# Performance work log

Measured on AMD Instinct MI355X. Metric: run time of the kernel, lower is better.

The kernel has to match this reference:

```python
import jax, jax.numpy as jnp
import numpy as np

B, C, H, W = 8, 256, 128, 128
WS, NH = 8, 8
HD = C // NH
HID = 4 * C
EPS = 1e-5


def _dwconv(x, w, b, pad):
    # x: [B,C,H,W], w: [C,1,k,k] depthwise
    y = jax.lax.conv_general_dilated(
        x, w, window_strides=(1, 1), padding=[(pad, pad), (pad, pad)],
        feature_group_count=C, dimension_numbers=('NCHW', 'OIHW', 'NCHW'))
    return y + b[None, :, None, None]


def _ln(x, g, b):
    m = jnp.mean(x, axis=-1, keepdims=True)
    v = jnp.mean(jnp.square(x - m), axis=-1, keepdims=True)
    return (x - m) * jax.lax.rsqrt(v + EPS) * g + b


def _mha(x, wqkv, bqkv, wo, bo):
    # x: [N,L,C]; torch nn.MultiheadAttention with q=k=v=x
    N, L, _ = x.shape
    qkv = x @ wqkv.T + bqkv
    q, k, v = jnp.split(qkv, 3, axis=-1)
    q = q.reshape(N, L, NH, HD)
    k = k.reshape(N, L, NH, HD)
    v = v.reshape(N, L, NH, HD)
    scale = HD ** -0.5
    a = jnp.einsum('nqhd,nkhd->nhqk', q * scale, k)
    a = jax.nn.softmax(a, axis=-1)
    o = jnp.einsum('nhqk,nkhd->nqhd', a, v).reshape(N, L, C)
    return o @ wo.T + bo


def _window_partition(x):
    b, c, h, w = x.shape
    x = x.reshape(b, c, h // WS, WS, w // WS, WS)
    return jnp.transpose(x, (0, 2, 4, 3, 5, 1)).reshape(-1, WS, WS, c)


def _window_reverse(win, h, w):
    c = win.shape[-1]
    x = win.reshape(-1, h // WS, w // WS, WS, WS, c)
    return jnp.transpose(x, (0, 5, 1, 3, 2, 4)).reshape(-1, c, h, w)


def _grid_partition(x):
    b, c, h, w = x.shape
    x = x.reshape(b, c, WS, h // WS, WS, w // WS)
    return jnp.transpose(x, (0, 3, 5, 2, 4, 1)).reshape(-1, WS, WS, c)


def _grid_reverse(grid, h, w):
    c = grid.shape[-1]
    x = grid.reshape(-1, h // WS, w // WS, WS, WS, c)
    return jnp.transpose(x, (0, 5, 2, 1, 3, 4)).reshape(-1, c, h, w)


def setup_inputs() -> dict:
    key = jax.random.key(0)
    ks = jax.random.split(key, 32)
    n = lambda k, s, sc=0.02: jax.random.normal(k, s, jnp.float32) * sc
    z = lambda s: jnp.zeros(s, jnp.float32)
    return {
        'x': jax.random.normal(ks[0], (B, C, H, W), jnp.float32),
        'w1': n(ks[1], (C, 1, 3, 3)), 'b1': z((C,)),
        'w2': n(ks[2], (C, 1, 5, 5)), 'b2': z((C,)),
        'w3': n(ks[3], (C, 1, 7, 7)), 'b3': z((C,)),
        'wf': n(ks[4], (C, 3 * C)), 'bf': z((C,)),
        'gw': jnp.ones((C,), jnp.float32), 'bw': z((C,)),
        'wqkv_w': n(ks[5], (3 * C, C)), 'bqkv_w': z((3 * C,)),
        'wo_w': n(ks[6], (C, C)), 'bo_w': z((C,)),
        'gg': jnp.ones((C,), jnp.float32), 'bg': z((C,)),
        'wqkv_g': n(ks[7], (3 * C, C)), 'bqkv_g': z((3 * C,)),
        'wo_g': n(ks[8], (C, C)), 'bo_g': z((C,)),
        'gm': jnp.ones((C,), jnp.float32), 'bm': z((C,)),
        'm1w': n(ks[9], (HID, C)), 'm1b': z((HID,)),
        'm2w': n(ks[10], (C, HID)), 'm2b': z((C,)),
    }


def reference(x, w1, b1, w2, b2, w3, b3, wf, bf, gw, bw, wqkv_w, bqkv_w, wo_w, bo_w,
              gg, bg, wqkv_g, bqkv_g, wo_g, bo_g, gm, bm, m1w, m1b, m2w, m2b):
    s1 = _dwconv(x, w1, b1, 1)
    s2 = _dwconv(x, w2, b2, 2)
    s3 = _dwconv(x, w3, b3, 3)
    cat = jnp.concatenate([s1, s2, s3], axis=1)  # [B,3C,H,W]
    x_multi = jnp.einsum('bkhw,ck->bchw', cat, wf) + bf[None, :, None, None]

    # window attention branch
    xw = _window_partition(x_multi).reshape(-1, WS * WS, C)
    xw = _ln(xw, gw, bw)
    xw = _mha(xw, wqkv_w, bqkv_w, wo_w, bo_w).reshape(-1, WS, WS, C)
    x = x + _window_reverse(xw, H, W)

    # grid attention branch
    xg = _grid_partition(x).reshape(-1, WS * WS, C)
    xg = _ln(xg, gg, bg)
    xg = _mha(xg, wqkv_g, bqkv_g, wo_g, bo_g).reshape(-1, WS, WS, C)
    x = x + _grid_reverse(xg, H, W)

    # MLP over flattened tokens
    xf = x.reshape(B, C, H * W).transpose(0, 2, 1)  # [B,HW,C]
    h = _ln(xf, gm, bm)
    h = jax.nn.gelu(h @ m1w.T + m1b, approximate=False)
    h = h @ m2w.T + m2b
    xf = xf + h
    return xf.transpose(0, 2, 1).reshape(B, C, H, W)
```

## Files before the change

kernel.cpp:

```cpp
#include <hip/hip_runtime.h>
#include <hip/hip_bf16.h>
#include <math.h>


#define CC 256
#define HH 128
#define WW 128
#define HWSZ 16384

typedef __attribute__((ext_vector_type(8))) short short8v;
typedef __attribute__((ext_vector_type(4))) float float4v;

#if defined(__has_builtin)
#if __has_builtin(__builtin_amdgcn_global_load_lds)
#define USE_GLDS 1
#endif
#endif
#ifndef USE_GLDS
#define USE_GLDS 0
#endif

static __device__ __forceinline__ float bf2f(unsigned short u) {
    union { float f; unsigned int i; } x; x.i = ((unsigned int)u) << 16; return x.f;
}
static __device__ __forceinline__ unsigned short f2bf(float f) {
    union { float f; unsigned int i; } x; x.f = f;
    unsigned int r = x.i + 0x7FFFu + ((x.i >> 16) & 1u);
    return (unsigned short)(r >> 16);
}
template<int FMT> static __device__ __forceinline__ float ldin(const void* p, size_t i) {
    if (FMT == 0) return bf2f(((const unsigned short*)p)[i]);
    return ((const float*)p)[i];
}

#if USE_GLDS
static __device__ __forceinline__ void gload16(const unsigned short* g, unsigned short* l) {
    __builtin_amdgcn_global_load_lds(
        (const __attribute__((address_space(1))) unsigned int*)g,
        (__attribute__((address_space(3))) unsigned int*)l, 16, 0, 0);
}
#endif

__global__ void probe_kernel(const unsigned short* x, int* flags) {
    __shared__ int mx[256];
    int m = 0;
    for (int i = threadIdx.x; i < 65536; i += 256) {
        int e = (x[i] >> 7) & 0xFF;
        m = m > e ? m : e;
    }
    mx[threadIdx.x] = m; __syncthreads();
    for (int s = 128; s > 0; s >>= 1) {
        if (threadIdx.x < s) mx[threadIdx.x] = mx[threadIdx.x] > mx[threadIdx.x + s] ? mx[threadIdx.x] : mx[threadIdx.x + s];
        __syncthreads();
    }
    if (threadIdx.x == 0) flags[0] = (mx[0] > 200) ? 1 : 0;
}
__global__ void report_ws_kernel(unsigned short* out, long long n, float code) {
    long long i = (long long)blockIdx.x * blockDim.x + threadIdx.x;
    const long long st = (long long)gridDim.x * blockDim.x;
    unsigned short c = f2bf(code);
    for (; i < n; i += st) out[i] = c;
}

#define WF_OFF   0
#define WQW_OFF  196608
#define WOW_OFF  393216
#define WQG_OFF  458752
#define WOG_OFF  655360
#define M1W_OFF  720896
#define M2W_OFF  983040
#define WTOT     1245184
#define BF_OFF   0
#define GW_OFF   256
#define BW_OFF   512
#define BQW_OFF  768
#define BOW_OFF  1536
#define GG_OFF   1792
#define BG_OFF   2048
#define BQG_OFF  2304
#define BOG_OFF  3072
#define GM_OFF   3328
#define BM_OFF   3584
#define M1B_OFF  3840
#define M2B_OFF  4864
#define BTOT     5120

template<int FMT>
__global__ __launch_bounds__(256) void convert_weights_kernel(
    const void* __restrict__ wf, const void* __restrict__ wqkv_w, const void* __restrict__ wo_w,
    const void* __restrict__ wqkv_g, const void* __restrict__ wo_g,
    const void* __restrict__ m1w, const void* __restrict__ m2w,
    unsigned short* __restrict__ out, const int* __restrict__ flags)
{
    if (flags[0] != FMT) return;
    int i = blockIdx.x * 256 + threadIdx.x;
    const int st = gridDim.x * 256;
    for (; i < WTOT; i += st) {
        const void* src; int off;
        if (i < WQW_OFF)      { src = wf;     off = i; }
        else if (i < WOW_OFF) { src = wqkv_w; off = i - WQW_OFF; }
        else if (i < WQG_OFF) { src = wo_w;   off = i - WOW_OFF; }
        else if (i < WOG_OFF) { src = wqkv_g; off = i - WQG_OFF; }
        else if (i < M1W_OFF) { src = wo_g;   off = i - WOG_OFF; }
        else if (i < M2W_OFF) { src = m1w;    off = i - M1W_OFF; }
        else                  { src = m2w;    off = i - M2W_OFF; }
        out[i] = (FMT == 0) ? ((const unsigned short*)src)[off]
                            : f2bf(((const float*)src)[off]);
    }
}

template<int FMT>
__global__ __launch_bounds__(256) void convert_bias_kernel(
    const void* bf_, const void* gw, const void* bw, const void* bqkv_w, const void* bo_w,
    const void* gg, const void* bg, const void* bqkv_g, const void* bo_g,
    const void* gm, const void* bm, const void* m1b, const void* m2b,
    float* __restrict__ out, const int* __restrict__ flags)
{
    if (flags[0] != FMT) return;
    int i = blockIdx.x * 256 + threadIdx.x;
    if (i >= BTOT) return;
    const void* src; int off;
    if (i < GW_OFF)        { src = bf_;    off = i; }
    else if (i < BW_OFF)   { src = gw;     off = i - GW_OFF; }
    else if (i < BQW_OFF)  { src = bw;     off = i - BW_OFF; }
    else if (i < BOW_OFF)  { src = bqkv_w; off = i - BQW_OFF; }
    else if (i < GG_OFF)   { src = bo_w;   off = i - BOW_OFF; }
    else if (i < BG_OFF)   { src = gg;     off = i - GG_OFF; }
    else if (i < BQG_OFF)  { src = bg;     off = i - BG_OFF; }
    else if (i < BOG_OFF)  { src = bqkv_g; off = i - BQG_OFF; }
    else if (i < GM_OFF)   { src = bo_g;   off = i - BOG_OFF; }
    else if (i < BM_OFF)   { src = gm;     off = i - GM_OFF; }
    else if (i < M1B_OFF)  { src = bm;     off = i - BM_OFF; }
    else if (i < M2B_OFF)  { src = m1b;    off = i - M1B_OFF; }
    else                   { src = m2b;    off = i - M2B_OFF; }
    out[i] = ldin<FMT>(src, off);
}

template<int FMT>
__global__ __launch_bounds__(256) void transpose_in_kernel(
    const void* __restrict__ in, float* __restrict__ out, const int* __restrict__ flags)
{
    if (flags[0] != FMT) return;
    __shared__ float tile[64][65];
    const int b  = blockIdx.z;
    const int s0 = blockIdx.x * 64;
    const int r0 = blockIdx.y * 64;
    const int tx = threadIdx.x & 63;
    const int ty = threadIdx.x >> 6;
    const size_t sb = (size_t)b * CC * HWSZ;
    float* dst = out + (size_t)b * HWSZ * CC;
#pragma unroll
    for (int rr = 0; rr < 16; ++rr) {
        int row = ty + rr * 4;
        tile[row][tx] = ldin<FMT>(in, sb + (size_t)(r0 + row) * HWSZ + s0 + tx);
    }
    __syncthreads();
#pragma unroll
    for (int rr = 0; rr < 16; ++rr) {
        int srow = ty + rr * 4;
        dst[(size_t)(s0 + srow) * CC + r0 + tx] = tile[tx][srow];
    }
}

template<int FMT>
__global__ __launch_bounds__(256) void transpose_out_kernel(
    const float* __restrict__ in, void* __restrict__ out, const int* __restrict__ flags)
{
    if (flags[0] != FMT) return;
    __shared__ float tile[64][65];
    const int b  = blockIdx.z;
    const int h0 = blockIdx.x * 64;
    const int c0 = blockIdx.y * 64;
    const int tx = threadIdx.x & 63;
    const int ty = threadIdx.x >> 6;
    const float* src = in + (size_t)b * HWSZ * CC;
    const size_t db = (size_t)b * CC * HWSZ;
#pragma unroll
    for (int rr = 0; rr < 16; ++rr) {
        int row = ty + rr * 4;
        tile[row][tx] = src[(size_t)(h0 + row) * CC + c0 + tx];
    }
    __syncthreads();
#pragma unroll
    for (int rr = 0; rr < 16; ++rr) {
        int crow = ty + rr * 4;
        size_t di = db + (size_t)(c0 + crow) * HWSZ + h0 + tx;
        float v = tile[tx][crow];
        if (FMT) ((float*)out)[di] = v;
        else ((unsigned short*)out)[di] = f2bf(v);
    }
}

template<int FMT>
__global__ __launch_bounds__(256) void dwconv_cat_kernel(
    const void* __restrict__ x,
    const void* __restrict__ w1, const void* __restrict__ b1,
    const void* __restrict__ w2, const void* __restrict__ b2,
    const void* __restrict__ w3, const void* __restrict__ b3,
    unsigned short* __restrict__ cat, int Mc, const int* __restrict__ flags)
{
    if (flags[0] != FMT) return;
    __shared__ float patch[14][140];
    __shared__ float wt[83];
    const int hb = blockIdx.x;
    const int c  = blockIdx.y;
    const int b  = blockIdx.z;
    const int tid = threadIdx.x;

    if (tid < 83) {
        float v;
        if (tid < 9)       v = ldin<FMT>(w1, c * 9 + tid);
        else if (tid < 34) v = ldin<FMT>(w2, c * 25 + (tid - 9));
        else               v = ldin<FMT>(w3, c * 49 + (tid - 34));
        wt[tid] = v;
    }
    const int h0 = hb * 8;
    const size_t xb = ((size_t)b * CC + c) * HWSZ;

    for (int i = tid; i < 448; i += 256) {
        const int r  = i >> 5;
        const int c4 = (i & 31) * 4;
        const int gh = h0 - 3 + r;
        float4 vv;
        if (gh >= 0 && gh < HH) {
            if (FMT == 0) {
                ushort4 u = *(const ushort4*)((const unsigned short*)x + xb + (size_t)gh * WW + c4);
                vv.x = bf2f(u.x); vv.y = bf2f(u.y); vv.z = bf2f(u.z); vv.w = bf2f(u.w);
            } else {
                vv = *(const float4*)((const float*)x + xb + (size_t)gh * WW + c4);
            }
        } else { vv.x = vv.y = vv.z = vv.w = 0.f; }
        *(float4*)&patch[r][c4 + 4] = vv;
    }
    for (int i = tid; i < 84; i += 256) {
        const int r = i / 6, j = i % 6;
        const int gh = h0 - 3 + r;
        const int gw = (j < 3) ? (j - 3) : (125 + j);
        float v = 0.f;
        if (gh >= 0 && gh < HH && gw >= 0 && gw < WW)
            v = ldin<FMT>(x, xb + (size_t)gh * WW + gw);
        patch[r][gw + 4] = v;
    }
    __syncthreads();

    const int w  = tid & 127;
    const int rb = (tid >> 7) * 4;
    const float bb1 = ldin<FMT>(b1, c), bb2 = ldin<FMT>(b2, c), bb3 = ldin<FMT>(b3, c);

#pragma unroll
    for (int ri = 0; ri < 4; ++ri) {
        const int row = rb + ri;
        const int pr  = row + 3;
        float s1 = bb1, s2 = bb2, s3 = bb3;
#pragma unroll
        for (int dy = -1; dy <= 1; ++dy)
#pragma unroll
            for (int dx = -1; dx <= 1; ++dx)
                s1 += patch[pr + dy][w + 4 + dx] * wt[(dy + 1) * 3 + (dx + 1)];
#pragma unroll
        for (int dy = -2; dy <= 2; ++dy)
#pragma unroll
            for (int dx = -2; dx <= 2; ++dx)
                s2 += patch[pr + dy][w + 4 + dx] * wt[9 + (dy + 2) * 5 + (dx + 2)];
#pragma unroll
        for (int dy = -3; dy <= 3; ++dy)
#pragma unroll
            for (int dx = -3; dx <= 3; ++dx)
                s3 += patch[pr + dy][w + 4 + dx] * wt[34 + (dy + 3) * 7 + (dx + 3)];

        const size_t m = (size_t)b * HWSZ + (size_t)(h0 + row) * WW + w;
        cat[(size_t)c * Mc + m]         = f2bf(s1);
        cat[(size_t)(256 + c) * Mc + m] = f2bf(s2);
        cat[(size_t)(512 + c) * Mc + m] = f2bf(s3);
    }
}

template<int ALAYOUT, int EPI>
__global__ __launch_bounds__(256) void gemm_mfma_kernel(
    const unsigned short* __restrict__ A, const unsigned short* __restrict__ Bw,
    const float* __restrict__ bias, void* __restrict__ Cout,
    int N, int K, int lda)
{
    constexpr int ASTR = ALAYOUT ? 72 : 64;
    __shared__ unsigned short As[128 * ASTR];
    __shared__ unsigned short Bs[128 * 64];
    const int tid  = threadIdx.x;
    const int lane = tid & 63;
    const int wv   = tid >> 6;
    const int wm   = (wv >> 1) * 64;
    const int wn   = (wv & 1) * 64;
    const int l15  = lane & 15;
    const int quad = lane >> 4;

    const int nbx = gridDim.x;
    const int nwg = nbx * gridDim.y;
    const int bid = blockIdx.y * nbx + blockIdx.x;
    const int swz = (bid & 7) * (nwg >> 3) + (bid >> 3);
    const int m0 = (swz / nbx) * 128;
    const int n0 = (swz % nbx) * 128;

    const int sr   = lane >> 3;
    const int scol = (lane & 7) * 8;

    float4v acc[4][4] = {};

    for (int k0 = 0; k0 < K; k0 += 64) {
        __syncthreads();
        if (ALAYOUT == 0) {
            const unsigned short* ga = A + (size_t)(m0 + wv * 32 + sr) * K + k0 + scol;
#pragma unroll
            for (int p = 0; p < 4; ++p) {
                unsigned short* lb = &As[(wv * 32 + p * 8) * 64];
#if USE_GLDS
                gload16(ga + (size_t)(p * 8) * K, lb);
#else
                *(short8v*)(lb + lane * 8) = *(const short8v*)(ga + (size_t)(p * 8) * K);
#endif
            }
        } else {
#pragma unroll
            for (int p = 0; p < 4; ++p) {
                const int k  = p * 16 + (tid >> 4);
                const int mm = (tid & 15) * 8;
                const unsigned short* g = A + (size_t)(k0 + k) * lda + m0 + mm;
                ushort4 va = *(const ushort4*)g;
                ushort4 vb = *(const ushort4*)(g + 4);
                As[(mm + 0) * 72 + k] = va.x; As[(mm + 1) * 72 + k] = va.y;
                As[(mm + 2) * 72 + k] = va.z; As[(mm + 3) * 72 + k] = va.w;
                As[(mm + 4) * 72 + k] = vb.x; As[(mm + 5) * 72 + k] = vb.y;
                As[(mm + 6) * 72 + k] = vb.z; As[(mm + 7) * 72 + k] = vb.w;
            }
        }
        {
            const unsigned short* gb = Bw + (size_t)(n0 + wv * 32 + sr) * K + k0 + scol;
#pragma unroll
            for (int p = 0; p < 4; ++p) {
                unsigned short* lb = &Bs[(wv * 32 + p * 8) * 64];
#if USE_GLDS
                gload16(gb + (size_t)(p * 8) * K, lb);
#else
                *(short8v*)(lb + lane * 8) = *(const short8v*)(gb + (size_t)(p * 8) * K);
#endif
            }
        }
#if USE_GLDS
        asm volatile("s_waitcnt vmcnt(0)" ::: "memory");
#endif
        __syncthreads();

#pragma unroll
        for (int ks = 0; ks < 64; ks += 32) {
            short8v af[4], bfv[4];
#pragma unroll
            for (int i = 0; i < 4; ++i)
                af[i] = *(const short8v*)&As[(wm + i * 16 + l15) * ASTR + ks + quad * 8];
#pragma unroll
            for (int i = 0; i < 4; ++i)
                bfv[i] = *(const short8v*)&Bs[(wn + i * 16 + l15) * 64 + ks + quad * 8];
#pragma unroll
            for (int mi = 0; mi < 4; ++mi)
#pragma unroll
                for (int ni = 0; ni < 4; ++ni)
                    acc[mi][ni] = __builtin_amdgcn_mfma_f32_16x16x32_bf16(
                        af[mi], bfv[ni], acc[mi][ni], 0, 0, 0);
        }
    }

    float bv[4];
#pragma unroll
    for (int ni = 0; ni < 4; ++ni) bv[ni] = bias[n0 + wn + ni * 16 + l15];

#pragma unroll
    for (int mi = 0; mi < 4; ++mi) {
#pragma unroll
        for (int r = 0; r < 4; ++r) {
            const size_t row = (size_t)(m0 + wm + mi * 16 + quad * 4 + r);
#pragma unroll
            for (int ni = 0; ni < 4; ++ni) {
                const int col = n0 + wn + ni * 16 + l15;
                float v = acc[mi][ni][r] + bv[ni];
                if (EPI == 0) {
                    ((unsigned short*)Cout)[row * N + col] = f2bf(v);
                } else if (EPI == 1) {
                    float g = 0.5f * v * (1.0f + erff(v * 0.70710678118654752f));
                    ((unsigned short*)Cout)[row * N + col] = f2bf(g);
                } else {
                    ((float*)Cout)[row * N + col] += v;
                }
            }
        }
    }
}

template<int FIN>
__global__ __launch_bounds__(256) void ln_kernel(
    const void* __restrict__ inv, const float* __restrict__ g,
    const float* __restrict__ b, unsigned short* __restrict__ out)
{
    const int lane = threadIdx.x & 63;
    const int wv   = threadIdx.x >> 6;
    const size_t m = (size_t)blockIdx.x * 4 + wv;
    const int c0 = lane * 4;
    float v[4];
    if (FIN == 0) {
        ushort4 u = *(const ushort4*)((const unsigned short*)inv + m * CC + c0);
        v[0] = bf2f(u.x); v[1] = bf2f(u.y); v[2] = bf2f(u.z); v[3] = bf2f(u.w);
    } else {
        float4 f = *(const float4*)((const float*)inv + m * CC + c0);
        v[0] = f.x; v[1] = f.y; v[2] = f.z; v[3] = f.w;
    }
    float s  = v[0] + v[1] + v[2] + v[3];
    float sq = v[0]*v[0] + v[1]*v[1] + v[2]*v[2] + v[3]*v[3];
#pragma unroll
    for (int off = 32; off > 0; off >>= 1) {
        s  += __shfl_xor(s,  off);
        sq += __shfl_xor(sq, off);
    }
    const float mean = s * 0.00390625f;
    float var = sq * 0.00390625f - mean * mean;
    if (var < 0.f) var = 0.f;
    const float rs = rsqrtf(var + 1e-5f);
    ushort4 o;
    o.x = f2bf((v[0] - mean) * rs * g[c0 + 0] + b[c0 + 0]);
    o.y = f2bf((v[1] - mean) * rs * g[c0 + 1] + b[c0 + 1]);
    o.z = f2bf((v[2] - mean) * rs * g[c0 + 2] + b[c0 + 2]);
    o.w = f2bf((v[3] - mean) * rs * g[c0 + 3] + b[c0 + 3]);
    *(ushort4*)(out + m * CC + c0) = o;
}

template<int MODE>
__global__ __launch_bounds__(256) void attn_kernel(
    const unsigned short* __restrict__ qkv, unsigned short* __restrict__ attn_out)
{
    __shared__ unsigned short q_lds[64 * 72];
    __shared__ unsigned short k_lds[64 * 72];
    __shared__ unsigned short v_lds[64 * 72];
    __shared__ unsigned short vt_lds[32 * 72];
    __shared__ unsigned short p_lds[64 * 72];

    const int tid  = threadIdx.x;
    const int lane = tid & 63;
    const int wv   = tid >> 6;
    const int l15  = lane & 15;
    const int quad = lane >> 4;
    const int wi   = blockIdx.x;
    const int b    = wi >> 8;
    const int rem  = wi & 255;
    const int i2   = rem >> 4;
    const int j2   = rem & 15;

    const float scale = 0.17677669529663687f;

    auto gt_read = [&](int tok) -> size_t {
        const int p = tok >> 3, qq = tok & 7;
        int h_r, w_r;
        if (MODE == 0) { h_r = i2 * 8 + p;  w_r = j2 * 8 + qq; }
        else           { h_r = p * 16 + i2; w_r = qq * 16 + j2; }
        return (size_t)b * HWSZ + (size_t)h_r * WW + w_r;
    };
    auto gt_write = [&](int tok) -> size_t {
        const int p = tok >> 3, qq = tok & 7;
        int h_w, w_w;
        if (MODE == 0) { h_w = i2 * 8 + p; w_w = j2 * 8 + qq; }
        else { h_w = j2 * 8 + (i2 >> 1); w_w = (i2 & 1) * 64 + p * 8 + qq; }
        return (size_t)b * HWSZ + (size_t)h_w * WW + w_w;
    };

    for (int g = 0; g < 4; ++g) {
        for (int v = tid; v < 512; v += 256) {
            const int tok = v >> 3;
            const int cg  = (v & 7) * 8;
            const unsigned short* src = qkv + gt_read(tok) * 768 + g * 64 + cg;
            *(short8v*)&q_lds[tok * 72 + cg] = *(const short8v*)(src);
            *(short8v*)&k_lds[tok * 72 + cg] = *(const short8v*)(src + 256);
            *(short8v*)&v_lds[tok * 72 + cg] = *(const short8v*)(src + 512);
        }
        __syncthreads();

#pragma unroll
        for (int hl = 0; hl < 2; ++hl) {
            {
                const int tok = lane;
                const int dg  = wv * 8;
                short8v vv = *(const short8v*)&v_lds[tok * 72 + hl * 32 + dg];
#pragma unroll
                for (int j = 0; j < 8; ++j)
                    vt_lds[(dg + j) * 72 + tok] = (unsigned short)vv[j];
            }

            short8v af = *(const short8v*)&q_lds[(16 * wv + l15) * 72 + hl * 32 + quad * 8];
            float4v s[4];
#pragma unroll
            for (int ni = 0; ni < 4; ++ni) {
                short8v bfv = *(const short8v*)&k_lds[(16 * ni + l15) * 72 + hl * 32 + quad * 8];
                float4v z = {};
                s[ni] = __builtin_amdgcn_mfma_f32_16x16x32_bf16(af, bfv, z, 0, 0, 0);
            }

#pragma unroll
            for (int r = 0; r < 4; ++r) {
                float m1 = fmaxf(fmaxf(s[0][r], s[1][r]), fmaxf(s[2][r], s[3][r]));
#pragma unroll
                for (int off = 1; off < 16; off <<= 1) m1 = fmaxf(m1, __shfl_xor(m1, off));
                const float rowmax = m1 * scale;
                float sum = 0.f;
#pragma unroll
                for (int ni = 0; ni < 4; ++ni) {
                    const float e = __expf(s[ni][r] * scale - rowmax);
                    s[ni][r] = e; sum += e;
                }
#pragma unroll
                for (int off = 1; off < 16; off <<= 1) sum += __shfl_xor(sum, off);
                const float inv = 1.f / sum;
#pragma unroll
                for (int ni = 0; ni < 4; ++ni) s[ni][r] *= inv;
            }

#pragma unroll
            for (int ni = 0; ni < 4; ++ni)
#pragma unroll
                for (int r = 0; r < 4; ++r)
                    p_lds[(16 * wv + quad * 4 + r) * 72 + ni * 16 + l15] = f2bf(s[ni][r]);

            __syncthreads();

            float4v o[2] = {};
#pragma unroll
            for (int kk = 0; kk < 2; ++kk) {
                short8v pf = *(const short8v*)&p_lds[(16 * wv + l15) * 72 + kk * 32 + quad * 8];
#pragma unroll
                for (int dt = 0; dt < 2; ++dt) {
                    short8v vf = *(const short8v*)&vt_lds[(dt * 16 + l15) * 72 + kk * 32 + quad * 8];
                    o[dt] = __builtin_amdgcn_mfma_f32_16x16x32_bf16(pf, vf, o[dt], 0, 0, 0);
                }
            }

            const int head = g * 2 + hl;
#pragma unroll
            for (int r = 0; r < 4; ++r) {
                const int tok = 16 * wv + quad * 4 + r;
                unsigned short* op = attn_out + gt_write(tok) * CC + head * 32;
                op[l15]      = f2bf(o[0][r]);
                op[16 + l15] = f2bf(o[1][r]);
            }
            __syncthreads();
        }
    }
}

extern "C" void kernel_launch(void* const* d_in, const int* in_sizes, int n_in,
                              void* d_out, int out_size, void* d_ws, size_t ws_size,
                              hipStream_t stream)
{
    const void* x      = d_in[0];
    const void* w1     = d_in[1];  const void* b1  = d_in[2];
    const void* w2     = d_in[3];  const void* b2  = d_in[4];
    const void* w3     = d_in[5];  const void* b3  = d_in[6];
    const void* wf     = d_in[7];  const void* bf_ = d_in[8];
    const void* gw     = d_in[9];  const void* bw  = d_in[10];
    const void* wqkv_w = d_in[11]; const void* bqkv_w = d_in[12];
    const void* wo_w   = d_in[13]; const void* bo_w   = d_in[14];
    const void* gg     = d_in[15]; const void* bg  = d_in[16];
    const void* wqkv_g = d_in[17]; const void* bqkv_g = d_in[18];
    const void* wo_g   = d_in[19]; const void* bo_g   = d_in[20];
    const void* gm     = d_in[21]; const void* bm  = d_in[22];
    const void* m1w    = d_in[23]; const void* m1b = d_in[24];
    const void* m2w    = d_in[25]; const void* m2b = d_in[26];

    const size_t MiB = 1048576ull;
    const long long nout = (long long)out_size;

    if (72 * MiB > ws_size) {
        float wsMiB = (float)(ws_size / MiB);
        if (wsMiB > 8192.f) wsMiB = 8192.f;
        report_ws_kernel<<<1024, 256, 0, stream>>>((unsigned short*)d_out, nout, 1024.f + wsMiB);
        return;
    }

    int nb = 8;
    while (nb > 1 && (size_t)nb * 64 * MiB + 8 * MiB > ws_size) nb >>= 1;
    const int nchunks = 8 / nb;
    const int Mc = nb * HWSZ;

    char* ws = (char*)d_ws;
    float*          xs   = (float*)ws;
    unsigned short* regA = (unsigned short*)(ws + (size_t)nb * 16 * MiB);
    unsigned short* xmat = (unsigned short*)(ws + (size_t)nb * 48 * MiB);
    unsigned short* xln  = (unsigned short*)(ws + (size_t)nb * 56 * MiB);
    int*            flags = (int*)(ws + (size_t)nb * 64 * MiB);
    unsigned short* wbf  = (unsigned short*)(ws + (size_t)nb * 64 * MiB + 1 * MiB);
    float*          bcv  = (float*)(ws + (size_t)nb * 64 * MiB + 4 * MiB);

    probe_kernel<<<1, 256, 0, stream>>>((const unsigned short*)x, flags);
    convert_weights_kernel<0><<<1024, 256, 0, stream>>>(wf, wqkv_w, wo_w, wqkv_g, wo_g, m1w, m2w, wbf, flags);
    convert_weights_kernel<1><<<1024, 256, 0, stream>>>(wf, wqkv_w, wo_w, wqkv_g, wo_g, m1w, m2w, wbf, flags);
    convert_bias_kernel<0><<<20, 256, 0, stream>>>(bf_, gw, bw, bqkv_w, bo_w, gg, bg, bqkv_g, bo_g, gm, bm, m1b, m2b, bcv, flags);
    convert_bias_kernel<1><<<20, 256, 0, stream>>>(bf_, gw, bw, bqkv_w, bo_w, gg, bg, bqkv_g, bo_g, gm, bm, m1b, m2b, bcv, flags);

    const int MB = Mc / 128;
    for (int c = 0; c < nchunks; ++c) {
        const size_t elemOff = (size_t)c * nb * CC * HWSZ;
        const void* xc0 = (const void*)((const unsigned short*)x + elemOff);
        const void* xc1 = (const void*)((const float*)x + elemOff);
        void* outc0 = (void*)((unsigned short*)d_out + elemOff);
        void* outc1 = (void*)((float*)d_out + elemOff);
        unsigned short* cat  = regA;
        unsigned short* qkvb = regA;
        unsigned short* h1   = regA;
        unsigned short* xm   = xmat;
        unsigned short* attn = xmat;

        transpose_in_kernel<0><<<dim3(256, 4, nb), 256, 0, stream>>>(xc0, xs, flags);
        transpose_in_kernel<1><<<dim3(256, 4, nb), 256, 0, stream>>>(xc1, xs, flags);

        dwconv_cat_kernel<0><<<dim3(16, 256, nb), 256, 0, stream>>>(xc0, w1, b1, w2, b2, w3, b3, cat, Mc, flags);
        dwconv_cat_kernel<1><<<dim3(16, 256, nb), 256, 0, stream>>>(xc1, w1, b1, w2, b2, w3, b3, cat, Mc, flags);

        gemm_mfma_kernel<1, 0><<<dim3(2, MB), 256, 0, stream>>>(cat, wbf + WF_OFF, bcv + BF_OFF, xm, 256, 768, Mc);

        ln_kernel<0><<<Mc / 4, 256, 0, stream>>>(xm, bcv + GW_OFF, bcv + BW_OFF, xln);
        gemm_mfma_kernel<0, 0><<<dim3(6, MB), 256, 0, stream>>>(xln, wbf + WQW_OFF, bcv + BQW_OFF, qkvb, 768, 256, 0);
        attn_kernel<0><<<nb * 256, 256, 0, stream>>>(qkvb, attn);
        gemm_mfma_kernel<0, 2><<<dim3(2, MB), 256, 0, stream>>>(attn, wbf + WOW_OFF, bcv + BOW_OFF, xs, 256, 256, 0);

        ln_kernel<1><<<Mc / 4, 256, 0, stream>>>(xs, bcv + GG_OFF, bcv + BG_OFF, xln);
        gemm_mfma_kernel<0, 0><<<dim3(6, MB), 256, 0, stream>>>(xln, wbf + WQG_OFF, bcv + BQG_OFF, qkvb, 768, 256, 0);
        attn_kernel<1><<<nb * 256, 256, 0, stream>>>(qkvb, attn);
        gemm_mfma_kernel<0, 2><<<dim3(2, MB), 256, 0, stream>>>(attn, wbf + WOG_OFF, bcv + BOG_OFF, xs, 256, 256, 0);

        ln_kernel<1><<<Mc / 4, 256, 0, stream>>>(xs, bcv + GM_OFF, bcv + BM_OFF, xln);
        gemm_mfma_kernel<0, 1><<<dim3(8, MB), 256, 0, stream>>>(xln, wbf + M1W_OFF, bcv + M1B_OFF, h1, 1024, 256, 0);
        gemm_mfma_kernel<0, 2><<<dim3(2, MB), 256, 0, stream>>>(h1, wbf + M2W_OFF, bcv + M2B_OFF, xs, 256, 1024, 0);

        transpose_out_kernel<0><<<dim3(256, 4, nb), 256, 0, stream>>>(xs, outc0, flags);
        transpose_out_kernel<1><<<dim3(256, 4, nb), 256, 0, stream>>>(xs, outc1, flags);
    }
}
```

Measured before the change: 1.842 ms.

## Register-block depthwise conv, vectorize transposes, preconvert dwconv weights to fp32 arena

The depthwise conv kernel now has each thread compute four adjacent outputs. It loads each 7-wide patch row once as float4 vectors and reuses those values across the 3x3, 5x5 and 7x7 filters, then writes ushort4 stores. Its weights and biases now come from a preconverted fp32 arena filled by the bias-conversion kernel, not from per-block shared-memory staging. The input and output transposes switch to 4-wide vector global loads and stores, which aims to cut memory instruction count. One risk is strided LDS accesses in the transposes, which may cause bank conflicts.

```diff
diff --git a/kernel.cpp b/kernel.cpp
--- a/kernel.cpp
+++ b/kernel.cpp
@@ -83,7 +83,13 @@
 #define BM_OFF   3584
 #define M1B_OFF  3840
 #define M2B_OFF  4864
-#define BTOT     5120
+#define DW1_OFF  5120
+#define DW2_OFF  7424
+#define DW3_OFF  13824
+#define DB1_OFF  26368
+#define DB2_OFF  26624
+#define DB3_OFF  26880
+#define BTOT     27136
 
 template<int FMT>
 __global__ __launch_bounds__(256) void convert_weights_kernel(
@@ -114,26 +120,36 @@
     const void* bf_, const void* gw, const void* bw, const void* bqkv_w, const void* bo_w,
     const void* gg, const void* bg, const void* bqkv_g, const void* bo_g,
     const void* gm, const void* bm, const void* m1b, const void* m2b,
+    const void* w1, const void* w2, const void* w3,
+    const void* b1, const void* b2, const void* b3,
     float* __restrict__ out, const int* __restrict__ flags)
 {
     if (flags[0] != FMT) return;
     int i = blockIdx.x * 256 + threadIdx.x;
-    if (i >= BTOT) return;
-    const void* src; int off;
-    if (i < GW_OFF)        { src = bf_;    off = i; }
-    else if (i < BW_OFF)   { src = gw;     off = i - GW_OFF; }
-    else if (i < BQW_OFF)  { src = bw;     off = i - BW_OFF; }
-    else if (i < BOW_OFF)  { src = bqkv_w; off = i - BQW_OFF; }
-    else if (i < GG_OFF)   { src = bo_w;   off = i - BOW_OFF; }
-    else if (i < BG_OFF)   { src = gg;     off = i - GG_OFF; }
-    else if (i < BQG_OFF)  { src = bg;     off = i - BG_OFF; }
-    else if (i < BOG_OFF)  { src = bqkv_g; off = i - BQG_OFF; }
-    else if (i < GM_OFF)   { src = bo_g;   off = i - BOG_OFF; }
-    else if (i < BM_OFF)   { src = gm;     off = i - GM_OFF; }
-    else if (i < M1B_OFF)  { src = bm;     off = i - BM_OFF; }
-    else if (i < M2B_OFF)  { src = m1b;    off = i - M1B_OFF; }
-    else                   { src = m2b;    off = i - M2B_OFF; }
-    out[i] = ldin<FMT>(src, off);
+    const int st = gridDim.x * 256;
+    for (; i < BTOT; i += st) {
+        const void* src; int off;
+        if (i < GW_OFF)        { src = bf_;    off = i; }
+        else if (i < BW_OFF)   { src = gw;     off = i - GW_OFF; }
+        else if (i < BQW_OFF)  { src = bw;     off = i - BW_OFF; }
+        else if (i < BOW_OFF)  { src = bqkv_w; off = i - BQW_OFF; }
+        else if (i < GG_OFF)   { src = bo_w;   off = i - BOW_OFF; }
+        else if (i < BG_OFF)   { src = gg;     off = i - GG_OFF; }
+        else if (i < BQG_OFF)  { src = bg;     off = i - BG_OFF; }
+        else if (i < BOG_OFF)  { src = bqkv_g; off = i - BQG_OFF; }
+        else if (i < GM_OFF)   { src = bo_g;   off = i - BOG_OFF; }
+        else if (i < BM_OFF)   { src = gm;     off = i - GM_OFF; }
+        else if (i < M1B_OFF)  { src = bm;     off = i - BM_OFF; }
+        else if (i < M2B_OFF)  { src = m1b;    off = i - M1B_OFF; }
+        else if (i < DW1_OFF)  { src = m2b;    off = i - M2B_OFF; }
+        else if (i < DW2_OFF)  { src = w1;     off = i - DW1_OFF; }
+        else if (i < DW3_OFF)  { src = w2;     off = i - DW2_OFF; }
+        else if (i < DB1_OFF)  { src = w3;     off = i - DW3_OFF; }
+        else if (i < DB2_OFF)  { src = b1;     off = i - DB1_OFF; }
+        else if (i < DB3_OFF)  { src = b2;     off = i - DB2_OFF; }
+        else                   { src = b3;     off = i - DB3_OFF; }
+        out[i] = ldin<FMT>(src, off);
+    }
 }
 
 template<int FMT>
@@ -149,10 +165,23 @@
     const int ty = threadIdx.x >> 6;
     const size_t sb = (size_t)b * CC * HWSZ;
     float* dst = out + (size_t)b * HWSZ * CC;
-#pragma unroll
-    for (int rr = 0; rr < 16; ++rr) {
-        int row = ty + rr * 4;
-        tile[row][tx] = ldin<FMT>(in, sb + (size_t)(r0 + row) * HWSZ + s0 + tx);
+
+    const int hw4 = (threadIdx.x & 15) * 4;
+    const int chb = threadIdx.x >> 4;
+#pragma unroll
+    for (int p = 0; p < 4; ++p) {
+        const int ch = chb + p * 16;
+        const size_t gi = sb + (size_t)(r0 + ch) * HWSZ + s0 + hw4;
+        float v0, v1, v2, v3;
+        if (FMT == 0) {
+            ushort4 u = *(const ushort4*)((const unsigned short*)in + gi);
+            v0 = bf2f(u.x); v1 = bf2f(u.y); v2 = bf2f(u.z); v3 = bf2f(u.w);
+        } else {
+            float4 f = *(const float4*)((const float*)in + gi);
+            v0 = f.x; v1 = f.y; v2 = f.z; v3 = f.w;
+        }
+        tile[ch][hw4] = v0; tile[ch][hw4 + 1] = v1;
+        tile[ch][hw4 + 2] = v2; tile[ch][hw4 + 3] = v3;
     }
     __syncthreads();
 #pragma unroll
@@ -171,49 +200,50 @@
     const int b  = blockIdx.z;
     const int h0 = blockIdx.x * 64;
     const int c0 = blockIdx.y * 64;
-    const int tx = threadIdx.x & 63;
-    const int ty = threadIdx.x >> 6;
     const float* src = in + (size_t)b * HWSZ * CC;
     const size_t db = (size_t)b * CC * HWSZ;
-#pragma unroll
-    for (int rr = 0; rr < 16; ++rr) {
-        int row = ty + rr * 4;
-        tile[row][tx] = src[(size_t)(h0 + row) * CC + c0 + tx];
+
+    const int ch4 = (threadIdx.x & 15) * 4;
+    const int hwb = threadIdx.x >> 4;
+#pragma unroll
+    for (int p = 0; p < 4; ++p) {
+        const int hw = hwb + p * 16;
+        float4 f = *(const float4*)(src + (size_t)(h0 + hw) * CC + c0 + ch4);
+        tile[hw][ch4] = f.x; tile[hw][ch4 + 1] = f.y;
+        tile[hw][ch4 + 2] = f.z; tile[hw][ch4 + 3] = f.w;
     }
     __syncthreads();
-#pragma unroll
-    for (int rr = 0; rr < 16; ++rr) {
-        int crow = ty + rr * 4;
-        size_t di = db + (size_t)(c0 + crow) * HWSZ + h0 + tx;
-        float v = tile[tx][crow];
-        if (FMT) ((float*)out)[di] = v;
-        else ((unsigned short*)out)[di] = f2bf(v);
+    const int hw4 = (threadIdx.x & 15) * 4;
+    const int chb = threadIdx.x >> 4;
+#pragma unroll
+    for (int p = 0; p < 4; ++p) {
+        const int ch = chb + p * 16;
+        const size_t di = db + (size_t)(c0 + ch) * HWSZ + h0 + hw4;
+        float v0 = tile[hw4][ch], v1 = tile[hw4 + 1][ch];
+        float v2 = tile[hw4 + 2][ch], v3 = tile[hw4 + 3][ch];
+        if (FMT) {
+            float4 f; f.x = v0; f.y = v1; f.z = v2; f.w = v3;
+            *(float4*)((float*)out + di) = f;
+        } else {
+            ushort4 u;
+            u.x = f2bf(v0); u.y = f2bf(v1); u.z = f2bf(v2); u.w = f2bf(v3);
+            *(ushort4*)((unsigned short*)out + di) = u;
+        }
     }
 }
 
 template<int FMT>
 __global__ __launch_bounds__(256) void dwconv_cat_kernel(
-    const void* __restrict__ x,
-    const void* __restrict__ w1, const void* __restrict__ b1,
-    const void* __restrict__ w2, const void* __restrict__ b2,
-    const void* __restrict__ w3, const void* __restrict__ b3,
+    const void* __restrict__ x, const float* __restrict__ arena,
     unsigned short* __restrict__ cat, int Mc, const int* __restrict__ flags)
 {
     if (flags[0] != FMT) return;
     __shared__ float patch[14][140];
-    __shared__ float wt[83];
     const int hb = blockIdx.x;
     const int c  = blockIdx.y;
     const int b  = blockIdx.z;
     const int tid = threadIdx.x;
 
-    if (tid < 83) {
-        float v;
-        if (tid < 9)       v = ldin<FMT>(w1, c * 9 + tid);
-        else if (tid < 34) v = ldin<FMT>(w2, c * 25 + (tid - 9));
-        else               v = ldin<FMT>(w3, c * 49 + (tid - 34));
-        wt[tid] = v;
-    }
     const int h0 = hb * 8;
     const size_t xb = ((size_t)b * CC + c) * HWSZ;
 
@@ -243,36 +273,59 @@
     }
     __syncthreads();
 
-    const int w  = tid & 127;
-    const int rb = (tid >> 7) * 4;
-    const float bb1 = ldin<FMT>(b1, c), bb2 = ldin<FMT>(b2, c), bb3 = ldin<FMT>(b3, c);
-
-#pragma unroll
-    for (int ri = 0; ri < 4; ++ri) {
-        const int row = rb + ri;
-        const int pr  = row + 3;
-        float s1 = bb1, s2 = bb2, s3 = bb3;
-#pragma unroll
-        for (int dy = -1; dy <= 1; ++dy)
-#pragma unroll
-            for (int dx = -1; dx <= 1; ++dx)
-                s1 += patch[pr + dy][w + 4 + dx] * wt[(dy + 1) * 3 + (dx + 1)];
-#pragma unroll
-        for (int dy = -2; dy <= 2; ++dy)
-#pragma unroll
-            for (int dx = -2; dx <= 2; ++dx)
-                s2 += patch[pr + dy][w + 4 + dx] * wt[9 + (dy + 2) * 5 + (dx + 2)];
-#pragma unroll
-        for (int dy = -3; dy <= 3; ++dy)
-#pragma unroll
-            for (int dx = -3; dx <= 3; ++dx)
-                s3 += patch[pr + dy][w + 4 + dx] * wt[34 + (dy + 3) * 7 + (dx + 3)];
-
-        const size_t m = (size_t)b * HWSZ + (size_t)(h0 + row) * WW + w;
-        cat[(size_t)c * Mc + m]         = f2bf(s1);
-        cat[(size_t)(256 + c) * Mc + m] = f2bf(s2);
-        cat[(size_t)(512 + c) * Mc + m] = f2bf(s3);
-    }
+    const int rowIdx = tid >> 5;
+    const int cb     = (tid & 31) * 4;
+
+    const float* wt1 = arena + DW1_OFF + c * 9;
+    const float* wt2 = arena + DW2_OFF + c * 25;
+    const float* wt3 = arena + DW3_OFF + c * 49;
+    const float bb1 = arena[DB1_OFF + c];
+    const float bb2 = arena[DB2_OFF + c];
+    const float bb3 = arena[DB3_OFF + c];
+
+    float s1[4] = {bb1, bb1, bb1, bb1};
+    float s2[4] = {bb2, bb2, bb2, bb2};
+    float s3[4] = {bb3, bb3, bb3, bb3};
+
+#pragma unroll
+    for (int r7 = 0; r7 < 7; ++r7) {
+        const int prow = rowIdx + r7;
+        float4 a = *(const float4*)&patch[prow][cb];
+        float4 d = *(const float4*)&patch[prow][cb + 4];
+        float4 e = *(const float4*)&patch[prow][cb + 8];
+        float vals[12] = {a.x, a.y, a.z, a.w, d.x, d.y, d.z, d.w, e.x, e.y, e.z, e.w};
+#pragma unroll
+        for (int dx7 = 0; dx7 < 7; ++dx7) {
+            const float wv = wt3[r7 * 7 + dx7];
+#pragma unroll
+            for (int wi = 0; wi < 4; ++wi) s3[wi] += vals[wi + dx7 + 1] * wv;
+        }
+        if (r7 >= 1 && r7 <= 5) {
+#pragma unroll
+            for (int dx5 = 0; dx5 < 5; ++dx5) {
+                const float wv = wt2[(r7 - 1) * 5 + dx5];
+#pragma unroll
+                for (int wi = 0; wi < 4; ++wi) s2[wi] += vals[wi + dx5 + 2] * wv;
+            }
+        }
+        if (r7 >= 2 && r7 <= 4) {
+#pragma unroll
+            for (int dx3 = 0; dx3 < 3; ++dx3) {
+                const float wv = wt1[(r7 - 2) * 3 + dx3];
+#pragma unroll
+                for (int wi = 0; wi < 4; ++wi) s1[wi] += vals[wi + dx3 + 3] * wv;
+            }
+        }
+    }
+
+    const size_t m = (size_t)b * HWSZ + (size_t)(h0 + rowIdx) * WW + cb;
+    ushort4 o1, o2, o3;
+    o1.x = f2bf(s1[0]); o1.y = f2bf(s1[1]); o1.z = f2bf(s1[2]); o1.w = f2bf(s1[3]);
+    o2.x = f2bf(s2[0]); o2.y = f2bf(s2[1]); o2.z = f2bf(s2[2]); o2.w = f2bf(s2[3]);
+    o3.x = f2bf(s3[0]); o3.y = f2bf(s3[1]); o3.z = f2bf(s3[2]); o3.w = f2bf(s3[3]);
+    *(ushort4*)&cat[(size_t)c * Mc + m]         = o1;
+    *(ushort4*)&cat[(size_t)(256 + c) * Mc + m] = o2;
+    *(ushort4*)&cat[(size_t)(512 + c) * Mc + m] = o3;
 }
 
 template<int ALAYOUT, int EPI>
@@ -594,8 +647,8 @@
     probe_kernel<<<1, 256, 0, stream>>>((const unsigned short*)x, flags);
     convert_weights_kernel<0><<<1024, 256, 0, stream>>>(wf, wqkv_w, wo_w, wqkv_g, wo_g, m1w, m2w, wbf, flags);
     convert_weights_kernel<1><<<1024, 256, 0, stream>>>(wf, wqkv_w, wo_w, wqkv_g, wo_g, m1w, m2w, wbf, flags);
-    convert_bias_kernel<0><<<20, 256, 0, stream>>>(bf_, gw, bw, bqkv_w, bo_w, gg, bg, bqkv_g, bo_g, gm, bm, m1b, m2b, bcv, flags);
-    convert_bias_kernel<1><<<20, 256, 0, stream>>>(bf_, gw, bw, bqkv_w, bo_w, gg, bg, bqkv_g, bo_g, gm, bm, m1b, m2b, bcv, flags);
+    convert_bias_kernel<0><<<106, 256, 0, stream>>>(bf_, gw, bw, bqkv_w, bo_w, gg, bg, bqkv_g, bo_g, gm, bm, m1b, m2b, w1, w2, w3, b1, b2, b3, bcv, flags);
+    convert_bias_kernel<1><<<106, 256, 0, stream>>>(bf_, gw, bw, bqkv_w, bo_w, gg, bg, bqkv_g, bo_g, gm, bm, m1b, m2b, w1, w2, w3, b1, b2, b3, bcv, flags);
 
     const int MB = Mc / 128;
     for (int c = 0; c < nchunks; ++c) {
@@ -613,8 +666,8 @@
         transpose_in_kernel<0><<<dim3(256, 4, nb), 256, 0, stream>>>(xc0, xs, flags);
         transpose_in_kernel<1><<<dim3(256, 4, nb), 256, 0, stream>>>(xc1, xs, flags);
 
-        dwconv_cat_kernel<0><<<dim3(16, 256, nb), 256, 0, stream>>>(xc0, w1, b1, w2, b2, w3, b3, cat, Mc, flags);
-        dwconv_cat_kernel<1><<<dim3(16, 256, nb), 256, 0, stream>>>(xc1, w1, b1, w2, b2, w3, b3, cat, Mc, flags);
+        dwconv_cat_kernel<0><<<dim3(16, 256, nb), 256, 0, stream>>>(xc0, bcv, cat, Mc, flags);
+        dwconv_cat_kernel<1><<<dim3(16, 256, nb), 256, 0, stream>>>(xc1, bcv, cat, Mc, flags);
 
         gemm_mfma_kernel<1, 0><<<dim3(2, MB), 256, 0, stream>>>(cat, wbf + WF_OFF, bcv + BF_OFF, xm, 256, 768, Mc);
 
```

After: 1.767 ms. -4.0%, faster.
